# Kernel tuning notes

Hardware: AMD Instinct MI355X
Metric: run time of the kernel (lower is better)

## Reference

```python
import jax, jax.numpy as jnp
import numpy as np

DILATIONS = (1, 6, 12, 24, 36)
EPS = 1e-5


def conv2d(x, w, dil, pad):
    # x: (N,C,H,W), w: (O,I,3,3) or (O,I,1,1)
    return jax.lax.conv_general_dilated(
        x, w, window_strides=(1, 1), padding=[(pad, pad), (pad, pad)],
        rhs_dilation=(dil, dil), dimension_numbers=('NCHW', 'OIHW', 'NCHW'))


def _bilinear_sample(img, ys, xs):
    # img: (C,H,W); ys, xs: (H,W,9) float sampling coords; zero padding outside.
    C, H, W = img.shape
    y0 = jnp.floor(ys)
    x0 = jnp.floor(xs)
    wy1 = ys - y0
    wx1 = xs - x0
    wy0 = 1.0 - wy1
    wx0 = 1.0 - wx1

    def gather(yi, xi, w):
        valid = (yi >= 0) & (yi < H) & (xi >= 0) & (xi < W)
        yc = jnp.clip(yi, 0, H - 1).astype(jnp.int32)
        xc = jnp.clip(xi, 0, W - 1).astype(jnp.int32)
        v = img[:, yc, xc]  # (C,H,W,9)
        return v * (w * valid)[None]

    return (gather(y0, x0, wy0 * wx0) + gather(y0, x0 + 1, wy0 * wx1)
            + gather(y0 + 1, x0, wy1 * wx0) + gather(y0 + 1, x0 + 1, wy1 * wx1))


def deform_unfold(x, offset, dil, pad):
    # x: (N,C,H,W), offset: (N,18,H,W) interleaved (dy,dx) per 3x3 tap.
    N, C, H, W = x.shape
    ky = jnp.repeat(jnp.arange(3), 3)  # (9,)
    kx = jnp.tile(jnp.arange(3), 3)
    base_y = (jnp.arange(H)[:, None, None] + (ky * dil - pad)).astype(x.dtype)  # (H,1,9)
    base_x = (jnp.arange(W)[None, :, None] + (kx * dil - pad)).astype(x.dtype)  # (1,W,9)
    dy = jnp.transpose(offset[:, 0::2], (0, 2, 3, 1))  # (N,H,W,9)
    dx = jnp.transpose(offset[:, 1::2], (0, 2, 3, 1))
    ys = base_y[None] + dy  # (N,H,W,9)
    xs = base_x[None] + dx
    return jax.vmap(_bilinear_sample)(x, ys, xs)  # (N,C,H,W,9)


def dynamic_head(x, cat_ws, scale_w, gamma, beta):
    N, C, H, W = x.shape
    outs = [x]
    for w, dil in zip(cat_ws, DILATIONS):
        fo = conv2d(x, w, dil, dil)           # (N,27,H,W); pad == dil keeps size
        filt = jax.nn.softmax(jnp.transpose(fo[:, :9], (0, 2, 3, 1)), axis=-1)  # (N,H,W,9)
        off = fo[:, -18:]                      # (N,18,H,W)
        samp = deform_unfold(x, off, dil, dil)  # (N,C,H,W,9)
        outs.append(jnp.einsum('nchwk,nhwk->nchw', samp, filt))
    cat = jnp.concatenate(outs, axis=1)        # (N,6C,H,W)
    y = conv2d(cat, scale_w, 1, 0)             # (N,C,H,W)
    mean = jnp.mean(y, axis=(0, 2, 3))
    var = jnp.var(y, axis=(0, 2, 3))
    y = (y - mean[None, :, None, None]) * jax.lax.rsqrt(var + EPS)[None, :, None, None]
    return y * gamma[None, :, None, None] + beta[None, :, None, None]


def setup_inputs() -> dict:
    key = jax.random.key(0)
    ks = jax.random.split(key, 8)
    C = 512
    x = jax.random.normal(ks[0], (2, C, 64, 64), dtype=jnp.float32)
    cat_ws = [0.02 * jax.random.normal(ks[1 + i], (27, C, 3, 3), dtype=jnp.float32) for i in range(5)]
    scale_w = 0.02 * jax.random.normal(ks[6], (C, 6 * C, 1, 1), dtype=jnp.float32)
    gamma = jnp.ones((C,), dtype=jnp.float32)
    beta = jnp.zeros((C,), dtype=jnp.float32)
    return {'x': x, 'w1': cat_ws[0], 'w2': cat_ws[1], 'w3': cat_ws[2],
            'w4': cat_ws[3], 'w5': cat_ws[4], 'scale_w': scale_w,
            'gamma': gamma, 'beta': beta}


def reference(x, w1, w2, w3, w4, w5, scale_w, gamma, beta):
    return dynamic_head(x, (w1, w2, w3, w4, w5), scale_w, gamma, beta)
```

## Files before the change

kernel.cpp:

```cpp
#include <hip/hip_runtime.h>

typedef short short8 __attribute__((ext_vector_type(8)));
typedef float f32x4 __attribute__((ext_vector_type(4)));

#define CST 3072

__device__ __forceinline__ float bf2f(short s) {
  unsigned u = ((unsigned)(unsigned short)s) << 16;
  return __builtin_bit_cast(float, u);
}
__device__ __forceinline__ short f2bf(float f) {
  unsigned u = __builtin_bit_cast(unsigned, f);
  u = (u + 0x7FFFu + ((u >> 16) & 1u)) >> 16;
  return (short)u;
}
__device__ __forceinline__ void gl16(const short* g, short* l) {
  __builtin_amdgcn_global_load_lds(
      (const __attribute__((address_space(1))) unsigned*)g,
      (__attribute__((address_space(3))) unsigned*)l, 16, 0, 0);
}

__global__ __launch_bounds__(256) void k_init(const float* __restrict__ x,
                                              const float* __restrict__ sw,
                                              const float* __restrict__ w1, const float* __restrict__ w2,
                                              const float* __restrict__ w3, const float* __restrict__ w4,
                                              const float* __restrict__ w5,
                                              short* __restrict__ cat,
                                              short* __restrict__ wbf, short* __restrict__ wdr,
                                              float* __restrict__ stats) {
  __shared__ float tile[64][65];
  int b = blockIdx.x;
  int t = threadIdx.x;
  if (b < 1024) {
    int cblk = b & 7, h = (b >> 3) & 63, n = b >> 9;
    int c0 = cblk * 64;
    int lw = t & 63, grp = t >> 6;
    const float* xp = x + (((size_t)n * 512 + c0) * 64 + h) * 64;
#pragma unroll
    for (int i = 0; i < 16; ++i) {
      int cl = grp * 16 + i;
      tile[cl][lw] = xp[(size_t)cl * 4096 + lw];
    }
    __syncthreads();
    int cl = t & 63;
    size_t mbase = ((size_t)n * 64 + h) * 64;
#pragma unroll
    for (int i = 0; i < 16; ++i) {
      int w = grp * 16 + i;
      cat[(mbase + w) * CST + c0 + cl] = f2bf(tile[cl][w]);
    }
  } else {
    int idx = (b - 1024) * 256 + t;
    const int NS = 512 * 3072;
    const int NW = 5 * 9 * 32 * 512;
    if (idx < NS) {
      wbf[idx] = f2bf(sw[idx]);
    } else if (idx < NS + NW) {
      int j = idx - NS;
      int c = j & 511;
      int t2 = j >> 9;
      int oc = t2 & 31;
      int t3 = t2 >> 5;
      int tap = t3 % 9;
      int di = t3 / 9;
      float v = 0.f;
      if (oc < 27) {
        const float* wp = (di == 0) ? w1 : (di == 1) ? w2 : (di == 2) ? w3 : (di == 3) ? w4 : w5;
        v = wp[((oc * 512 + c) * 3 + tap / 3) * 3 + tap % 3];
      }
      wdr[j] = f2bf(v);
    } else if (idx < NS + NW + 1024) {
      stats[idx - NS - NW] = 0.f;
    }
  }
}

__global__ __launch_bounds__(128) void k_conv(const short* __restrict__ xsrc,
                                              const short* __restrict__ wdr_all,
                                              int* __restrict__ ctab) {
  __shared__ short As[64 * 256];
  __shared__ short Bs[32 * 256];
  float (*fo)[32][33] = (float (*)[32][33])(void*)As;
  int tid = threadIdx.x;
  int wave = tid >> 6, lane = tid & 63;
  int l15 = lane & 15, quad = lane >> 4;
  int b = blockIdx.x;
  int di = b >> 7;
  int loc = b & 127;
  const int DIL[5] = {1, 6, 12, 24, 36};
  int d = DIL[di];
  int rid = (loc & 7) * 16 + (loc >> 3);
  int h = rid & 63, n = rid >> 6;
  f32x4 acc[2][2];
  f32x4 zz = {0.f, 0.f, 0.f, 0.f};
#pragma unroll
  for (int i = 0; i < 2; ++i)
#pragma unroll
    for (int j = 0; j < 2; ++j) acc[i][j] = zz;
  const short8 z8 = {0, 0, 0, 0, 0, 0, 0, 0};
  int aoff[16];
  int boff[8];
#pragma unroll
  for (int i = 0; i < 16; ++i) {
    int q = i * 128 + tid;
    int w = q >> 5, ch = q & 31;
    aoff[i] = w * CST + (ch ^ (w & 7)) * 8;
  }
#pragma unroll
  for (int i = 0; i < 8; ++i) {
    int q = i * 128 + tid;
    int oc = q >> 5, ch = q & 31;
    boff[i] = oc * 512 + (ch ^ (oc & 7)) * 8;
  }
  const short* wbase = wdr_all + (size_t)di * 9 * 32 * 512;
  int rowb = (n << 12);
#pragma unroll 1
  for (int kh = 0; kh < 2; ++kh) {
    int lastty = -1;
#pragma unroll
    for (int tap = 0; tap < 9; ++tap) {
      int ty = tap / 3, tx = tap % 3;
      int hh = h + (ty - 1) * d;
      if ((unsigned)hh >= 64u) continue;
      __syncthreads();
      if (ty != lastty) {
        const short* abase = xsrc + (size_t)(rowb + (hh << 6)) * CST + kh * 256;
#pragma unroll
        for (int i = 0; i < 16; ++i)
          gl16(abase + aoff[i], As + (i * 128 + wave * 64) * 8);
        lastty = ty;
      }
      {
        const short* bbase = wbase + tap * 32 * 512 + kh * 256;
#pragma unroll
        for (int i = 0; i < 8; ++i)
          gl16(bbase + boff[i], Bs + (i * 128 + wave * 64) * 8);
      }
      __syncthreads();
      int s0 = wave * 32 + (tx - 1) * d;
#pragma unroll
      for (int ks = 0; ks < 8; ++ks) {
        int c = ks * 4 + quad;
        short8 a[2], bb[2];
#pragma unroll
        for (int mt = 0; mt < 2; ++mt) {
          int wp = s0 + mt * 16 + l15;
          bool ok = (unsigned)wp < 64u;
          int wc = ok ? wp : 0;
          short8 av = *(const short8*)(As + wc * 256 + (c ^ (wc & 7)) * 8);
          a[mt] = ok ? av : z8;
        }
#pragma unroll
        for (int ot = 0; ot < 2; ++ot) {
          int oc = ot * 16 + l15;
          bb[ot] = *(const short8*)(Bs + oc * 256 + (c ^ (oc & 7)) * 8);
        }
#pragma unroll
        for (int mt = 0; mt < 2; ++mt)
#pragma unroll
          for (int ot = 0; ot < 2; ++ot)
            acc[mt][ot] = __builtin_amdgcn_mfma_f32_16x16x32_bf16(a[mt], bb[ot], acc[mt][ot], 0, 0, 0);
      }
    }
  }
  __syncthreads();
#pragma unroll
  for (int mt = 0; mt < 2; ++mt)
#pragma unroll
    for (int ot = 0; ot < 2; ++ot)
#pragma unroll
      for (int r = 0; r < 4; ++r)
        fo[wave][mt * 16 + quad * 4 + r][ot * 16 + l15] = acc[mt][ot][r];
  __syncthreads();
  if (tid < 64) {
    int p = tid;
    float* fp = fo[p >> 5][p & 31];
    float mx = fp[0];
#pragma unroll
    for (int k = 1; k < 9; ++k) mx = fmaxf(mx, fp[k]);
    float s = 0.f, e[9];
#pragma unroll
    for (int k = 0; k < 9; ++k) { e[k] = __expf(fp[k] - mx); s += e[k]; }
    float inv = 1.f / s;
#pragma unroll
    for (int k = 0; k < 9; ++k) fp[k] = e[k] * inv;
  }
  __syncthreads();
#pragma unroll
  for (int rr = 0; rr < 5; ++rr) {
    int task = rr * 128 + tid;
    if (task < 576) {
      int p = task / 9;
      int k = task - p * 9;
      const float* fp = fo[p >> 5][p & 31];
      float f = fp[k];
      float dy = fp[9 + 2 * k];
      float dx = fp[10 + 2 * k];
      float ys = (float)(h + (k / 3 - 1) * d) + dy;
      float xs = (float)(p + (k % 3 - 1) * d) + dx;
      float y0f = floorf(ys), x0f = floorf(xs);
      float wy1 = ys - y0f, wx1 = xs - x0f;
      float wy0 = 1.f - wy1, wx0 = 1.f - wx1;
      int y0 = (int)y0f, x0 = (int)x0f;
      int4 ent;
      int* ep = (int*)&ent;
#pragma unroll
      for (int cy = 0; cy < 2; ++cy)
#pragma unroll
        for (int cx = 0; cx < 2; ++cx) {
          int yy = y0 + cy, xx = x0 + cx;
          bool v = ((unsigned)yy < 64u) && ((unsigned)xx < 64u);
          float wt = f * (cy ? wy1 : wy0) * (cx ? wx1 : wx0);
          int row = v ? (yy * 64 + xx) : 0;
          unsigned wb = v ? (unsigned)(unsigned short)f2bf(wt) : 0u;
          ep[cy * 2 + cx] = row | (int)(wb << 16);
        }
      int mm = rowb + (h << 6) + p;
      ((int4*)ctab)[((size_t)di * 8192 + mm) * 9 + k] = ent;
    }
  }
}

__global__ __launch_bounds__(256, 4) void k_samp(const short* __restrict__ xsrc,
                                                 short* __restrict__ cat,
                                                 const int* __restrict__ ctab) {
  int tid = threadIdx.x;
  int wv = __builtin_amdgcn_readfirstlane(tid >> 6);
  int lane = tid & 63;
  int b = blockIdx.x;
  int di = b >> 11;
  int loc = b & 2047;
  int m = (loc & 7) * 1024 + (loc >> 3) * 4 + wv;
  int n = m >> 12;
  const int4* tp = (const int4*)ctab + ((size_t)di * 8192 + m) * 9;
  const short* xb = xsrc + (size_t)(n << 12) * CST + lane * 8;
  float acc[8] = {0.f, 0.f, 0.f, 0.f, 0.f, 0.f, 0.f, 0.f};
#pragma unroll
  for (int k = 0; k < 9; ++k) {
    int4 e = tp[k];
    const int* ep = (const int*)&e;
#pragma unroll
    for (int c = 0; c < 4; ++c) {
      int dw = ep[c];
      float wt = __builtin_bit_cast(float, (unsigned)dw & 0xFFFF0000u);
      int row = dw & 0xFFFF;
      const short8 vv = *(const short8*)(xb + (size_t)row * CST);
#pragma unroll
      for (int j = 0; j < 8; ++j) acc[j] += wt * bf2f(vv[j]);
    }
  }
  short8 o8;
#pragma unroll
  for (int j = 0; j < 8; ++j) o8[j] = f2bf(acc[j]);
  *(short8*)(cat + (size_t)m * CST + 512 * (di + 1) + lane * 8) = o8;
}

__global__ __launch_bounds__(256) void k_gemm(const short* __restrict__ A,
                                              const short* __restrict__ B,
                                              short* __restrict__ Y) {
  __shared__ short As[128 * 64];
  __shared__ short Bs[128 * 64];
  int tid = threadIdx.x;
  int wave = tid >> 6, lane = tid & 63;
  int l15 = lane & 15, quad = lane >> 4;
  int bid = blockIdx.x;
  int xcd = bid & 7, s = bid >> 3;
  int mt = xcd * 8 + (s >> 3);
  int nz = s & 7;
  int nt = nz & 3, kh = nz >> 2;
  int m0 = mt * 128, n0 = nt * 128;
  int kbeg = kh * 1536;
  int wm = (wave >> 1) * 64, wn = (wave & 1) * 64;
  f32x4 acc[4][4];
  f32x4 zz = {0.f, 0.f, 0.f, 0.f};
#pragma unroll
  for (int i = 0; i < 4; ++i)
#pragma unroll
    for (int j = 0; j < 4; ++j) acc[i][j] = zz;
  const short* agp[4];
  const short* bgp[4];
  short* adst[4];
  short* bdst[4];
#pragma unroll
  for (int it = 0; it < 4; ++it) {
    int q = it * 256 + tid;
    int row = q >> 3;
    int c8g = (q & 7) ^ (row & 7);
    agp[it] = A + (size_t)(m0 + row) * CST + kbeg + c8g * 8;
    bgp[it] = B + (size_t)(n0 + row) * CST + kbeg + c8g * 8;
    adst[it] = As + q * 8;
    bdst[it] = Bs + q * 8;
  }
  int slotbA = (wm + l15) & 7;
  int slotbB = (wn + l15) & 7;
#pragma unroll 1
  for (int ks = 0; ks < 24; ++ks) {
    int ko = ks * 64;
    __syncthreads();
#pragma unroll
    for (int it = 0; it < 4; ++it) gl16(agp[it] + ko, adst[it]);
#pragma unroll
    for (int it = 0; it < 4; ++it) gl16(bgp[it] + ko, bdst[it]);
    __syncthreads();
#pragma unroll
    for (int kk = 0; kk < 2; ++kk) {
      int sa = ((quad + kk * 4) ^ slotbA) * 8;
      int sb = ((quad + kk * 4) ^ slotbB) * 8;
      short8 af[4], bf[4];
#pragma unroll
      for (int i = 0; i < 4; ++i)
        af[i] = *(const short8*)(As + (wm + i * 16 + l15) * 64 + sa);
#pragma unroll
      for (int j = 0; j < 4; ++j)
        bf[j] = *(const short8*)(Bs + (wn + j * 16 + l15) * 64 + sb);
#pragma unroll
      for (int i = 0; i < 4; ++i)
#pragma unroll
        for (int j = 0; j < 4; ++j)
          acc[i][j] = __builtin_amdgcn_mfma_f32_16x16x32_bf16(af[i], bf[j], acc[i][j], 0, 0, 0);
    }
  }
  short* Yp = Y + (size_t)kh * (8192 * 512);
#pragma unroll
  for (int i = 0; i < 4; ++i) {
    int row = m0 + wm + i * 16 + quad * 4;
#pragma unroll
    for (int j = 0; j < 4; ++j) {
      int col = n0 + wn + j * 16 + l15;
#pragma unroll
      for (int r = 0; r < 4; ++r)
        Yp[(size_t)(row + r) * 512 + col] = f2bf(acc[i][j][r]);
    }
  }
}

__global__ __launch_bounds__(256) void k_stats(const short* __restrict__ Y,
                                               float* __restrict__ stats) {
  const short* Y1 = Y + (size_t)8192 * 512;
  int tid = threadIdx.x;
  int mb = blockIdx.x * 32;
  float s0 = 0.f, q0 = 0.f, s1 = 0.f, q1 = 0.f;
  for (int r = 0; r < 32; ++r) {
    size_t ro = (size_t)(mb + r) * 512;
    float v0 = bf2f(Y[ro + tid]) + bf2f(Y1[ro + tid]);
    float v1 = bf2f(Y[ro + tid + 256]) + bf2f(Y1[ro + tid + 256]);
    s0 += v0; q0 += v0 * v0;
    s1 += v1; q1 += v1 * v1;
  }
  atomicAdd(&stats[tid], s0);
  atomicAdd(&stats[tid + 256], s1);
  atomicAdd(&stats[512 + tid], q0);
  atomicAdd(&stats[512 + tid + 256], q1);
}

__global__ __launch_bounds__(256) void k_norm(const short* __restrict__ Y,
                                              const float* __restrict__ stats,
                                              const float* __restrict__ gamma,
                                              const float* __restrict__ beta,
                                              float* __restrict__ out) {
  __shared__ float tile[64][65];
  const short* Y1 = Y + (size_t)8192 * 512;
  int b = blockIdx.x;
  int cblk = b & 7, h = (b >> 3) & 63, n = b >> 9;
  int c0 = cblk * 64;
  int t = threadIdx.x;
  int cl = t & 63, grp = t >> 6;
  int c = c0 + cl;
  float mean = stats[c] * (1.f / 8192.f);
  float var = stats[512 + c] * (1.f / 8192.f) - mean * mean;
  float Ai = gamma[c] * rsqrtf(var + 1e-5f);
  float Bi = beta[c] - mean * Ai;
  size_t mbase = ((size_t)n * 64 + h) * 64;
#pragma unroll
  for (int i = 0; i < 16; ++i) {
    int w = grp * 16 + i;
    size_t ro = (mbase + w) * 512 + c;
    tile[w][cl] = (bf2f(Y[ro]) + bf2f(Y1[ro])) * Ai + Bi;
  }
  __syncthreads();
  float* op = out + (((size_t)n * 512 + c0) * 64 + h) * 64;
#pragma unroll
  for (int i = 0; i < 16; ++i) {
    int c2 = grp * 16 + i;
    op[(size_t)c2 * 4096 + cl] = tile[cl][c2];
  }
}

extern "C" void kernel_launch(void* const* d_in, const int* in_sizes, int n_in,
                              void* d_out, int out_size, void* d_ws, size_t ws_size,
                              hipStream_t stream) {
  const float* x  = (const float*)d_in[0];
  const float* w1 = (const float*)d_in[1];
  const float* w2 = (const float*)d_in[2];
  const float* w3 = (const float*)d_in[3];
  const float* w4 = (const float*)d_in[4];
  const float* w5 = (const float*)d_in[5];
  const float* sw = (const float*)d_in[6];
  const float* gamma = (const float*)d_in[7];
  const float* beta  = (const float*)d_in[8];
  float* out = (float*)d_out;

  char* ws = (char*)d_ws;
  short* cat   = (short*)ws;
  short* wbf   = (short*)(ws + 50331648);
  short* wdr   = (short*)(ws + 53477376);
  short* yb    = (short*)(ws + 54951936);
  float* stats = (float*)(ws + 71729152);
  int*   ctab  = (int*)(ws + 71733248);

  k_init<<<10052, 256, 0, stream>>>(x, sw, w1, w2, w3, w4, w5, cat, wbf, wdr, stats);
  k_conv<<<640, 128, 0, stream>>>(cat, wdr, ctab);
  k_samp<<<10240, 256, 0, stream>>>(cat, cat, ctab);
  k_gemm<<<512, 256, 0, stream>>>(cat, wbf, yb);
  k_stats<<<256, 256, 0, stream>>>(yb, stats);
  k_norm<<<1024, 256, 0, stream>>>(yb, stats, gamma, beta, out);
}
```

Measured before the change: 211.1 us.

## Double-buffer GEMM LDS tiles with split-phase prefetch and larger 128x256 blocks

Measured after the change: 213.2 us. About the same (+1.0%).

```diff
diff --git a/kernel.cpp b/kernel.cpp
--- a/kernel.cpp
+++ b/kernel.cpp
@@ -255,72 +255,116 @@
   *(short8*)(cat + (size_t)m * CST + 512 * (di + 1) + lane * 8) = o8;
 }
 
-__global__ __launch_bounds__(256) void k_gemm(const short* __restrict__ A,
-                                              const short* __restrict__ B,
-                                              short* __restrict__ Y) {
-  __shared__ short As[128 * 64];
-  __shared__ short Bs[128 * 64];
+__global__ __launch_bounds__(512, 2) void k_gemm(const short* __restrict__ A,
+                                                 const short* __restrict__ B,
+                                                 short* __restrict__ Y) {
+  __shared__ short As[2][128 * 64];
+  __shared__ short Bs[2][256 * 64];
   int tid = threadIdx.x;
   int wave = tid >> 6, lane = tid & 63;
   int l15 = lane & 15, quad = lane >> 4;
   int bid = blockIdx.x;
-  int xcd = bid & 7, s = bid >> 3;
-  int mt = xcd * 8 + (s >> 3);
-  int nz = s & 7;
-  int nt = nz & 3, kh = nz >> 2;
-  int m0 = mt * 128, n0 = nt * 128;
-  int kbeg = kh * 1536;
-  int wm = (wave >> 1) * 64, wn = (wave & 1) * 64;
+  int xcd = bid & 7, g = bid >> 3;
+  int mt = xcd * 8 + (g & 7);
+  int nt = (g >> 3) & 1;
+  int s  = g >> 4;
+  int m0 = mt * 128, n0 = nt * 256;
+  int kbeg = s * 1536;
+  int wm = (wave >> 2) * 64;
+  int wn = (wave & 3) * 64;
   f32x4 acc[4][4];
   f32x4 zz = {0.f, 0.f, 0.f, 0.f};
 #pragma unroll
   for (int i = 0; i < 4; ++i)
 #pragma unroll
     for (int j = 0; j < 4; ++j) acc[i][j] = zz;
-  const short* agp[4];
-  const short* bgp[4];
-  short* adst[4];
-  short* bdst[4];
-#pragma unroll
-  for (int it = 0; it < 4; ++it) {
-    int q = it * 256 + tid;
-    int row = q >> 3;
-    int c8g = (q & 7) ^ (row & 7);
-    agp[it] = A + (size_t)(m0 + row) * CST + kbeg + c8g * 8;
-    bgp[it] = B + (size_t)(n0 + row) * CST + kbeg + c8g * 8;
-    adst[it] = As + q * 8;
-    bdst[it] = Bs + q * 8;
-  }
-  int slotbA = (wm + l15) & 7;
-  int slotbB = (wn + l15) & 7;
+  int r6 = tid >> 3, c8 = tid & 7;
+  int cs = (c8 ^ (r6 & 7)) * 8;
+  const short* asrc = A + (size_t)(m0 + r6) * CST + kbeg + cs;
+  const short* bsrc = B + (size_t)(n0 + r6) * CST + kbeg + cs;
+  short* adst = &As[0][0] + tid * 8;
+  short* bdst = &Bs[0][0] + tid * 8;
+#define STAGE_A(p, u, kc) gl16(asrc + (size_t)(u) * 64 * CST + (kc), adst + (p) * 8192 + (u) * 4096)
+#define STAGE_B(p, u, kc) gl16(bsrc + (size_t)(u) * 64 * CST + (kc), bdst + (p) * 16384 + (u) * 4096)
+  STAGE_A(0, 0, 0); STAGE_A(0, 1, 0);
+  STAGE_B(0, 0, 0); STAGE_B(0, 1, 0); STAGE_B(0, 2, 0); STAGE_B(0, 3, 0);
+  STAGE_A(1, 0, 64); STAGE_A(1, 1, 64);
+  STAGE_B(1, 0, 64); STAGE_B(1, 1, 64); STAGE_B(1, 2, 64); STAGE_B(1, 3, 64);
 #pragma unroll 1
-  for (int ks = 0; ks < 24; ++ks) {
-    int ko = ks * 64;
-    __syncthreads();
-#pragma unroll
-    for (int it = 0; it < 4; ++it) gl16(agp[it] + ko, adst[it]);
-#pragma unroll
-    for (int it = 0; it < 4; ++it) gl16(bgp[it] + ko, bdst[it]);
-    __syncthreads();
-#pragma unroll
-    for (int kk = 0; kk < 2; ++kk) {
-      int sa = ((quad + kk * 4) ^ slotbA) * 8;
-      int sb = ((quad + kk * 4) ^ slotbB) * 8;
-      short8 af[4], bf[4];
+  for (int t = 0; t < 24; ++t) {
+    int cur = t & 1;
+    if (t == 23) { asm volatile("s_waitcnt vmcnt(0)" ::: "memory"); }
+    else         { asm volatile("s_waitcnt vmcnt(6)" ::: "memory"); }
+    __builtin_amdgcn_s_barrier();
+    __builtin_amdgcn_sched_barrier(0);
+    const short* Ab = &As[cur][0];
+    const short* Bb = &Bs[cur][0];
+    short8 a[4][2], bl[2][2];
+#pragma unroll
+    for (int i = 0; i < 4; ++i) {
+      int row = wm + i * 16 + l15;
+      const short* rp = Ab + row * 64;
+#pragma unroll
+      for (int kk = 0; kk < 2; ++kk)
+        a[i][kk] = *(const short8*)(rp + ((quad + kk * 4) ^ (row & 7)) * 8);
+    }
+#pragma unroll
+    for (int j = 0; j < 2; ++j) {
+      int row = wn + j * 16 + l15;
+      const short* rp = Bb + row * 64;
+#pragma unroll
+      for (int kk = 0; kk < 2; ++kk)
+        bl[j][kk] = *(const short8*)(rp + ((quad + kk * 4) ^ (row & 7)) * 8);
+    }
+    __builtin_amdgcn_s_barrier();
+    asm volatile("s_waitcnt lgkmcnt(0)" ::: "memory");
+    __builtin_amdgcn_sched_barrier(0);
+    __builtin_amdgcn_s_setprio(1);
+#pragma unroll
+    for (int kk = 0; kk < 2; ++kk)
 #pragma unroll
       for (int i = 0; i < 4; ++i)
-        af[i] = *(const short8*)(As + (wm + i * 16 + l15) * 64 + sa);
-#pragma unroll
-      for (int j = 0; j < 4; ++j)
-        bf[j] = *(const short8*)(Bs + (wn + j * 16 + l15) * 64 + sb);
+#pragma unroll
+        for (int j = 0; j < 2; ++j)
+          acc[i][j] = __builtin_amdgcn_mfma_f32_16x16x32_bf16(a[i][kk], bl[j][kk], acc[i][j], 0, 0, 0);
+    __builtin_amdgcn_s_setprio(0);
+    __builtin_amdgcn_s_barrier();
+    __builtin_amdgcn_sched_barrier(0);
+    short8 bh[2][2];
+#pragma unroll
+    for (int j = 0; j < 2; ++j) {
+      int row = wn + 32 + j * 16 + l15;
+      const short* rp = Bb + row * 64;
+#pragma unroll
+      for (int kk = 0; kk < 2; ++kk)
+        bh[j][kk] = *(const short8*)(rp + ((quad + kk * 4) ^ (row & 7)) * 8);
+    }
+    if (t < 22) {
+      int kc = (t + 2) * 64;
+      STAGE_A(cur, 0, kc); STAGE_A(cur, 1, kc);
+    }
+    __builtin_amdgcn_s_barrier();
+    asm volatile("s_waitcnt lgkmcnt(0)" ::: "memory");
+    __builtin_amdgcn_sched_barrier(0);
+    __builtin_amdgcn_s_setprio(1);
+#pragma unroll
+    for (int kk = 0; kk < 2; ++kk)
 #pragma unroll
       for (int i = 0; i < 4; ++i)
 #pragma unroll
-        for (int j = 0; j < 4; ++j)
-          acc[i][j] = __builtin_amdgcn_mfma_f32_16x16x32_bf16(af[i], bf[j], acc[i][j], 0, 0, 0);
-    }
-  }
-  short* Yp = Y + (size_t)kh * (8192 * 512);
+        for (int j = 0; j < 2; ++j)
+          acc[i][j + 2] = __builtin_amdgcn_mfma_f32_16x16x32_bf16(a[i][kk], bh[j][kk], acc[i][j + 2], 0, 0, 0);
+    __builtin_amdgcn_s_setprio(0);
+    __builtin_amdgcn_s_barrier();
+    __builtin_amdgcn_sched_barrier(0);
+    if (t < 22) {
+      int kc = (t + 2) * 64;
+      STAGE_B(cur, 0, kc); STAGE_B(cur, 1, kc); STAGE_B(cur, 2, kc); STAGE_B(cur, 3, kc);
+    }
+  }
+#undef STAGE_A
+#undef STAGE_B
+  short* Yp = Y + (size_t)s * (8192 * 512);
 #pragma unroll
   for (int i = 0; i < 4; ++i) {
     int row = m0 + wm + i * 16 + quad * 4;
@@ -411,7 +455,7 @@
   k_init<<<10052, 256, 0, stream>>>(x, sw, w1, w2, w3, w4, w5, cat, wbf, wdr, stats);
   k_conv<<<640, 128, 0, stream>>>(cat, wdr, ctab);
   k_samp<<<10240, 256, 0, stream>>>(cat, cat, ctab);
-  k_gemm<<<512, 256, 0, stream>>>(cat, wbf, yb);
+  k_gemm<<<256, 512, 0, stream>>>(cat, wbf, yb);
   k_stats<<<256, 256, 0, stream>>>(yb, stats);
   k_norm<<<1024, 256, 0, stream>>>(yb, stats, gamma, beta, out);
 }
```
